# Optimization experiments

Hardware: AMD Instinct MI355X
Metric: run time of the kernel (lower is better)

The kernel has to match this reference:

```python
import jax, jax.numpy as jnp
import numpy as np

SPD_EPS = 1e-3   # added to covariance diagonal
RE_EPS = 1e-4    # ReEig eigenvalue floor


def _semi_orth(key, d_out, d_in):
    # random point on Stiefel manifold: rows orthonormal (d_out <= d_in)
    a = jax.random.normal(key, (d_in, d_out), dtype=jnp.float32)
    q, _ = jnp.linalg.qr(a)          # (d_in, d_out), orthonormal columns
    return q.T                        # (d_out, d_in)


def setup_inputs() -> dict:
    key = jax.random.key(0)
    k_x, k_w1, k_w2, k_fc, k_b = jax.random.split(key, 5)
    B, C, T = 512, 128, 1000
    d1, d2, n_classes = 64, 32, 10
    x = jax.random.normal(k_x, (B, C, T), dtype=jnp.float32)
    W1 = _semi_orth(k_w1, d1, C)          # BiMap 1: (64, 128)
    W2 = _semi_orth(k_w2, d2, d1)         # BiMap 2: (32, 64)
    feat = d2 * d2
    fc_w = jax.random.normal(k_fc, (n_classes, feat), dtype=jnp.float32) / np.sqrt(feat)
    fc_b = jax.random.normal(k_b, (n_classes,), dtype=jnp.float32) * 0.01
    return {"x": x, "W1": W1, "W2": W2, "fc_w": fc_w, "fc_b": fc_b}


def _bimap(S, W):
    # W S W^T, batched: (B,d_in,d_in) -> (B,d_out,d_out)
    return jnp.einsum('ij,bjk,lk->bil', W, S, W)


def _eig_fn(S, fn):
    # eigendecompose symmetric S, apply fn to eigenvalues, reconstruct
    w, V = jnp.linalg.eigh(S)                       # (B,d), (B,d,d)
    return jnp.einsum('bij,bj,bkj->bik', V, fn(w), V)


def reference(x, W1, W2, fc_w, fc_b):
    B, C, T = x.shape
    # per-trial covariance
    x_c = x - x.mean(axis=2, keepdims=True)
    cov = jnp.einsum('bct,bdt->bcd', x_c, x_c) / (T - 1)
    cov = cov + SPD_EPS * jnp.eye(C, dtype=x.dtype)
    # BiMap -> ReEig (x2), then LogEig
    S = _bimap(cov, W1)
    S = _eig_fn(S, lambda w: jnp.maximum(w, RE_EPS))
    S = _bimap(S, W2)
    S = _eig_fn(S, lambda w: jnp.maximum(w, RE_EPS))
    S = _eig_fn(S, jnp.log)
    feats = S.reshape(B, -1)
    return feats @ fc_w.T + fc_b
```

## Files before the change

kernel.cpp:

```cpp
#include <hip/hip_runtime.h>
#include <hip/hip_bf16.h>
#include <math.h>

#define TN 1000
#define SPD_EPS 1e-3f

#define M0 1.16f
#define R0 0.86f
#define BETA 0.7413793103f

typedef float f32x16 __attribute__((ext_vector_type(16)));
typedef short bf16x8 __attribute__((ext_vector_type(8)));

__global__ void w21_kernel(const float* __restrict__ W2, const float* __restrict__ W1,
                           float* __restrict__ W21) {
  int idx = blockIdx.x * 256 + threadIdx.x;
  if (idx < 32 * 128) {
    int c = idx >> 7, k = idx & 127;
    float acc = 0.f;
#pragma unroll 8
    for (int m = 0; m < 64; ++m) acc += W2[c * 64 + m] * W1[m * 128 + k];
    W21[idx] = acc;
  }
}

__device__ __forceinline__ int tix(int r, int c) {
  return r * 4 - (r * (r - 1)) / 2 + (c - r);
}

__global__ __launch_bounds__(256) void cov_kernel(const float* __restrict__ x,
                                                  const float* __restrict__ W21,
                                                  float* __restrict__ S2) {
  const int b = blockIdx.x;
  const int tid = threadIdx.x;
  const int w = tid >> 6;
  const int l = tid & 63;
  const int ch = l & 31;
  const int h = l >> 5;

  __shared__ float Ct[10 * 1056];
  __shared__ float Pl[32 * 130];
  __shared__ float s_part[4][128];
  __shared__ float s_sh[128];

  for (int idx = tid; idx < 10 * 1056; idx += 256) Ct[idx] = 0.f;

  f32x16 acc00{}, acc01{}, acc02{}, acc03{}, acc11{}, acc12{}, acc13{},
         acc22{}, acc23{}, acc33{};
  float s_own[4] = {0.f, 0.f, 0.f, 0.f};
  bf16x8 fr[4];
  const float* xb = x + (size_t)b * (128 * TN) + (size_t)ch * TN + h * 8;
  float4 sa[8], sb[8];
  const float4 z4 = make_float4(0.f, 0.f, 0.f, 0.f);

#define LOADS(ST, KK) do {                                                   \
    const bool v_ = (16 * (KK) + 8 * h) < TN;                                \
    _Pragma("unroll")                                                        \
    for (int r_ = 0; r_ < 4; ++r_) {                                         \
      const float* p_ = xb + r_ * 32 * TN + 16 * (KK);                       \
      float4 t0_ = z4, t1_ = z4;                                             \
      if (v_) { t0_ = *(const float4*)p_; t1_ = *(const float4*)(p_ + 4); }  \
      ST[2 * r_] = t0_; ST[2 * r_ + 1] = t1_;                                \
    } } while (0)

#define CONVS(ST) do {                                                       \
    _Pragma("unroll")                                                        \
    for (int r_ = 0; r_ < 4; ++r_) {                                         \
      union { bf16x8 v; __hip_bfloat16 e[8]; } u_;                           \
      const float f_[8] = {ST[2*r_].x, ST[2*r_].y, ST[2*r_].z, ST[2*r_].w,   \
                           ST[2*r_+1].x, ST[2*r_+1].y, ST[2*r_+1].z,         \
                           ST[2*r_+1].w};                                    \
      float ss_ = 0.f;                                                       \
      _Pragma("unroll")                                                      \
      for (int i_ = 0; i_ < 8; ++i_) {                                       \
        u_.e[i_] = __float2bfloat16(f_[i_]); ss_ += f_[i_];                  \
      }                                                                      \
      fr[r_] = u_.v; s_own[r_] += ss_;                                       \
    } } while (0)

#define MFMAS() do {                                                         \
    acc00 = __builtin_amdgcn_mfma_f32_32x32x16_bf16(fr[0], fr[0], acc00, 0, 0, 0); \
    acc01 = __builtin_amdgcn_mfma_f32_32x32x16_bf16(fr[0], fr[1], acc01, 0, 0, 0); \
    acc02 = __builtin_amdgcn_mfma_f32_32x32x16_bf16(fr[0], fr[2], acc02, 0, 0, 0); \
    acc03 = __builtin_amdgcn_mfma_f32_32x32x16_bf16(fr[0], fr[3], acc03, 0, 0, 0); \
    acc11 = __builtin_amdgcn_mfma_f32_32x32x16_bf16(fr[1], fr[1], acc11, 0, 0, 0); \
    acc12 = __builtin_amdgcn_mfma_f32_32x32x16_bf16(fr[1], fr[2], acc12, 0, 0, 0); \
    acc13 = __builtin_amdgcn_mfma_f32_32x32x16_bf16(fr[1], fr[3], acc13, 0, 0, 0); \
    acc22 = __builtin_amdgcn_mfma_f32_32x32x16_bf16(fr[2], fr[2], acc22, 0, 0, 0); \
    acc23 = __builtin_amdgcn_mfma_f32_32x32x16_bf16(fr[2], fr[3], acc23, 0, 0, 0); \
    acc33 = __builtin_amdgcn_mfma_f32_32x32x16_bf16(fr[3], fr[3], acc33, 0, 0, 0); \
  } while (0)

  LOADS(sa, w);
#pragma unroll 1
  for (int s = w; s < 63; s += 8) {
    LOADS(sb, s + 4); CONVS(sa); MFMAS();
    LOADS(sa, s + 8); CONVS(sb); MFMAS();
  }

#pragma unroll
  for (int r = 0; r < 4; ++r) s_own[r] += __shfl_xor(s_own[r], 32);
  if (h == 0) {
#pragma unroll
    for (int r = 0; r < 4; ++r) s_part[w][32 * r + ch] = s_own[r];
  }
  __syncthreads();
  if (tid < 128)
    s_sh[tid] = s_part[0][tid] + s_part[1][tid] + s_part[2][tid] + s_part[3][tid];

#define ADD_T(ACC_) do {                                                     \
    float* tp_ = Ct + tlc * 1056;                                            \
    _Pragma("unroll")                                                        \
    for (int p_ = 0; p_ < 16; ++p_) {                                        \
      const int row_ = (p_ & 3) + 8 * (p_ >> 2) + 4 * h;                     \
      tp_[row_ * 33 + ch] += ACC_[p_];                                       \
    } } while (0)

#pragma unroll
  for (int s = 0; s < 10; ++s) {
    const int tlc = (s + 3 * w) % 10;
    switch (tlc) {
      case 0: ADD_T(acc00); break;
      case 1: ADD_T(acc01); break;
      case 2: ADD_T(acc02); break;
      case 3: ADD_T(acc03); break;
      case 4: ADD_T(acc11); break;
      case 5: ADD_T(acc12); break;
      case 6: ADD_T(acc13); break;
      case 7: ADD_T(acc22); break;
      case 8: ADD_T(acc23); break;
      case 9: ADD_T(acc33); break;
    }
    __syncthreads();
  }

  {
    const int RB[10] = {0, 0, 0, 0, 1, 1, 1, 2, 2, 3};
    const int CB[10] = {0, 1, 2, 3, 1, 2, 3, 2, 3, 3};
#pragma unroll
    for (int tl = 0; tl < 10; ++tl) {
#pragma unroll
      for (int e0 = 0; e0 < 1024; e0 += 256) {
        const int e = e0 + tid;
        const int row = e >> 5, col = e & 31;
        const int Rg = RB[tl] * 32 + row, Cg = CB[tl] * 32 + col;
        float cv = (Ct[tl * 1056 + row * 33 + col]
                    - s_sh[Rg] * s_sh[Cg] * (1.f / TN)) * (1.f / (TN - 1));
        if (Rg == Cg) cv += SPD_EPS;
        Ct[tl * 1056 + row * 33 + col] = cv;
      }
    }
  }
  __syncthreads();

  {
    const int j = tid & 127;
    const int rh = tid >> 7;
    const int cblk = j >> 5;
    float pa[16];
#pragma unroll
    for (int i = 0; i < 16; ++i) pa[i] = 0.f;
#pragma unroll
    for (int kb = 0; kb < 4; ++kb) {
      const bool up = (kb <= cblk);
      const int t1 = up ? tix(kb, cblk) : tix(cblk, kb);
      const int base = t1 * 1056 + (up ? (j & 31) : (j & 31) * 33);
      const int st = up ? 33 : 1;
      const float* wp = W21 + kb * 32;
#pragma unroll 1
      for (int k2 = 0; k2 < 32; ++k2) {
        const float cv = Ct[base + k2 * st];
#pragma unroll
        for (int i = 0; i < 16; ++i)
          pa[i] = fmaf(wp[(rh * 16 + i) * 128 + k2], cv, pa[i]);
      }
    }
#pragma unroll
    for (int i = 0; i < 16; ++i) Pl[(rh * 16 + i) * 130 + j] = pa[i];
  }
  __syncthreads();

  {
    const int ch2 = tid & 31;
    const int rg = tid >> 5;
    float sc[4] = {0.f, 0.f, 0.f, 0.f};
    const float* wr = W21 + ch2 * 128;
#pragma unroll 1
    for (int k = 0; k < 128; ++k) {
      const float wv = wr[k];
#pragma unroll
      for (int i = 0; i < 4; ++i)
        sc[i] = fmaf(Pl[(rg * 4 + i) * 130 + k], wv, sc[i]);
    }
    float* So = S2 + ((size_t)b << 10);
#pragma unroll
    for (int i = 0; i < 4; ++i) So[(rg * 4 + i) * 32 + ch2] = sc[i];
  }
}

__device__ __forceinline__ void mm_half(float* __restrict__ c,
                                        const float (* __restrict__ A)[36],
                                        const float* __restrict__ bf,
                                        const int r0) {
#pragma unroll 4
  for (int i = 0; i < 16; ++i) {
    const float4* row = (const float4*)(A[r0 + i]);
    float acc = 0.f;
#pragma unroll
    for (int kk = 0; kk < 8; ++kk) {
      const float4 r = row[kk];
      acc = fmaf(r.x, bf[4 * kk + 0], acc);
      acc = fmaf(r.y, bf[4 * kk + 1], acc);
      acc = fmaf(r.z, bf[4 * kk + 2], acc);
      acc = fmaf(r.w, bf[4 * kk + 3], acc);
    }
    c[i] = acc;
  }
}

__device__ __forceinline__ void expand32(float* __restrict__ bf,
                                         const float* __restrict__ v,
                                         const int h) {
#pragma unroll
  for (int i = 0; i < 16; ++i) {
    const float mine = v[i];
    const float other = __shfl_xor(mine, 32);
    bf[i]      = h ? other : mine;
    bf[i + 16] = h ? mine  : other;
  }
}

__global__ __launch_bounds__(64) void logm_fc_kernel(const float* __restrict__ S,
                                                     const float* __restrict__ fcw,
                                                     const float* __restrict__ fcb,
                                                     float* __restrict__ out) {
  const int b = blockIdx.x;
  const int l = threadIdx.x;
  const int j = l & 31;
  const int h = l >> 5;
  const int r0 = h << 4;
  const bool hd = ((j >> 4) == h);
  const int id = j & 15;

  __shared__ float P[6][32][36];
  __shared__ float a_sh[44];

  if (l < 42) {
    if (l == 0) a_sh[0] = logf(M0);
    else a_sh[l] = ((l & 1) ? 1.f : -1.f) * __powf(BETA, (float)l) / (float)l;
  }

  float cur[16], nxt[16], acc[16], bf[32];
  const float* Sb = S + ((size_t)b << 10);
#pragma unroll
  for (int i = 0; i < 16; ++i) {
    float v = Sb[(r0 + i) * 32 + j] * (1.f / R0);
    if (hd && i == id) v -= (M0 / R0);
    cur[i] = v;
    P[0][r0 + i][j] = v;
  }
  __syncthreads();

#pragma unroll 1
  for (int p = 1; p < 6; ++p) {
    expand32(bf, cur, h);
    mm_half(nxt, P[0], bf, r0);
#pragma unroll
    for (int i = 0; i < 16; ++i) { cur[i] = nxt[i]; P[p][r0 + i][j] = nxt[i]; }
  }
  __syncthreads();

#pragma unroll
  for (int i = 0; i < 16; ++i) {
    float v = (hd && i == id) ? a_sh[36] : 0.f;
#pragma unroll
    for (int p = 0; p < 5; ++p)
      v = fmaf(a_sh[37 + p], P[p][r0 + i][j], v);
    acc[i] = v;
  }
#pragma unroll 1
  for (int jj = 5; jj >= 0; --jj) {
    expand32(bf, acc, h);
    mm_half(nxt, P[5], bf, r0);
#pragma unroll
    for (int i = 0; i < 16; ++i) {
      float v = (hd && i == id) ? a_sh[6 * jj] : 0.f;
#pragma unroll
      for (int p = 0; p < 5; ++p)
        v = fmaf(a_sh[6 * jj + 1 + p], P[p][r0 + i][j], v);
      acc[i] = v + nxt[i];
    }
  }

#pragma unroll 2
  for (int k = 0; k < 10; ++k) {
    const float* fw = fcw + (size_t)k * 1024;
    float s = 0.f;
#pragma unroll
    for (int i = 0; i < 16; ++i)
      s = fmaf(acc[i], fw[(r0 + i) * 32 + j], s);
#pragma unroll
    for (int d = 1; d < 64; d <<= 1) s += __shfl_xor(s, d);
    if (l == 0) out[b * 10 + k] = s + fcb[k];
  }
}

extern "C" void kernel_launch(void* const* d_in, const int* in_sizes, int n_in,
                              void* d_out, int out_size, void* d_ws, size_t ws_size,
                              hipStream_t stream) {
  const float* x   = (const float*)d_in[0];
  const float* W1  = (const float*)d_in[1];
  const float* W2  = (const float*)d_in[2];
  const float* fcw = (const float*)d_in[3];
  const float* fcb = (const float*)d_in[4];
  float* out = (float*)d_out;
  char* ws = (char*)d_ws;
  float* W21 = (float*)ws;
  float* S2  = (float*)(ws + 65536);

  w21_kernel<<<16, 256, 0, stream>>>(W2, W1, W21);
  cov_kernel<<<512, 256, 0, stream>>>(x, W21, S2);
  logm_fc_kernel<<<512, 64, 0, stream>>>(S2, fcw, fcb, out);
}
```

Baseline: 171.7 us.

## Stage x tiles through double-buffered LDS with coalesced loads before MFMA covariance

Previously each lane loaded two float4s from per-channel rows in its MFMA fragment layout, so a wavefront touched 32 scattered rows per load. The new code has each wave load 32 full rows of 64-sample chunks with coalesced float4 loads. It converts them to bf16 into a double-buffered LDS tile, computes row sums with shuffles, and then reads MFMA fragments back from LDS. This is meant to improve global memory coalescing and overlap the next chunk's load with MFMA work, at the cost of LDS traffic, a block barrier per chunk, and a shared smem union reused for the covariance tile.

```diff
diff --git a/kernel.cpp b/kernel.cpp
--- a/kernel.cpp
+++ b/kernel.cpp
@@ -28,6 +28,10 @@
   return r * 4 - (r * (r - 1)) / 2 + (c - r);
 }
 
+#define YS_STR 68
+#define YS_ELE (128 * 68)
+#define PL_OFF 42240
+
 __global__ __launch_bounds__(256) void cov_kernel(const float* __restrict__ x,
                                                   const float* __restrict__ W21,
                                                   float* __restrict__ S2) {
@@ -37,45 +41,48 @@
   const int l = tid & 63;
   const int ch = l & 31;
   const int h = l >> 5;
-
-  __shared__ float Ct[10 * 1056];
-  __shared__ float Pl[32 * 130];
-  __shared__ float s_part[4][128];
-  __shared__ float s_sh[128];
-
-  for (int idx = tid; idx < 10 * 1056; idx += 256) Ct[idx] = 0.f;
+  const int g = l & 15;
+  const int rr = l >> 4;
+
+  __shared__ __align__(16) char smem[58880];
+  __shared__ float s_acc[128];
+  ushort* ys = (ushort*)smem;
+  float* Ct = (float*)smem;
+  float* Pl = (float*)(smem + PL_OFF);
+
+  if (tid < 128) s_acc[tid] = 0.f;
 
   f32x16 acc00{}, acc01{}, acc02{}, acc03{}, acc11{}, acc12{}, acc13{},
          acc22{}, acc23{}, acc33{};
-  float s_own[4] = {0.f, 0.f, 0.f, 0.f};
   bf16x8 fr[4];
-  const float* xb = x + (size_t)b * (128 * TN) + (size_t)ch * TN + h * 8;
-  float4 sa[8], sb[8];
+  float4 st[8];
+  const float* xb = x + (size_t)b * (128 * TN);
   const float4 z4 = make_float4(0.f, 0.f, 0.f, 0.f);
 
-#define LOADS(ST, KK) do {                                                   \
-    const bool v_ = (16 * (KK) + 8 * h) < TN;                                \
+#define CLOAD(TT) do {                                                       \
+    const int t0_ = (TT) * 64;                                               \
+    const bool v_ = (4 * g) < (TN - t0_);                                    \
     _Pragma("unroll")                                                        \
-    for (int r_ = 0; r_ < 4; ++r_) {                                         \
-      const float* p_ = xb + r_ * 32 * TN + 16 * (KK);                       \
-      float4 t0_ = z4, t1_ = z4;                                             \
-      if (v_) { t0_ = *(const float4*)p_; t1_ = *(const float4*)(p_ + 4); }  \
-      ST[2 * r_] = t0_; ST[2 * r_ + 1] = t1_;                                \
+    for (int rg_ = 0; rg_ < 8; ++rg_) {                                      \
+      const int R_ = 32 * w + 4 * rg_ + rr;                                  \
+      st[rg_] = v_ ? *(const float4*)(xb + (size_t)R_ * TN + t0_ + 4 * g)    \
+                   : z4;                                                     \
     } } while (0)
 
-#define CONVS(ST) do {                                                       \
+#define CSTORE(BUF) do {                                                     \
+    ushort* yb_ = ys + (BUF) * YS_ELE;                                       \
     _Pragma("unroll")                                                        \
-    for (int r_ = 0; r_ < 4; ++r_) {                                         \
-      union { bf16x8 v; __hip_bfloat16 e[8]; } u_;                           \
-      const float f_[8] = {ST[2*r_].x, ST[2*r_].y, ST[2*r_].z, ST[2*r_].w,   \
-                           ST[2*r_+1].x, ST[2*r_+1].y, ST[2*r_+1].z,         \
-                           ST[2*r_+1].w};                                    \
-      float ss_ = 0.f;                                                       \
-      _Pragma("unroll")                                                      \
-      for (int i_ = 0; i_ < 8; ++i_) {                                       \
-        u_.e[i_] = __float2bfloat16(f_[i_]); ss_ += f_[i_];                  \
-      }                                                                      \
-      fr[r_] = u_.v; s_own[r_] += ss_;                                       \
+    for (int rg_ = 0; rg_ < 8; ++rg_) {                                      \
+      const int R_ = 32 * w + 4 * rg_ + rr;                                  \
+      const float4 v_ = st[rg_];                                             \
+      float sm_ = v_.x + v_.y + v_.z + v_.w;                                 \
+      sm_ += __shfl_xor(sm_, 1); sm_ += __shfl_xor(sm_, 2);                  \
+      sm_ += __shfl_xor(sm_, 4); sm_ += __shfl_xor(sm_, 8);                  \
+      if (g == 0) s_acc[R_] += sm_;                                          \
+      union { ushort4 q; __hip_bfloat16 e[4]; } u_;                          \
+      u_.e[0] = __float2bfloat16(v_.x); u_.e[1] = __float2bfloat16(v_.y);    \
+      u_.e[2] = __float2bfloat16(v_.z); u_.e[3] = __float2bfloat16(v_.w);    \
+      *(ushort4*)(yb_ + R_ * YS_STR + 4 * g) = u_.q;                         \
     } } while (0)
 
 #define MFMAS() do {                                                         \
@@ -91,22 +98,33 @@
     acc33 = __builtin_amdgcn_mfma_f32_32x32x16_bf16(fr[3], fr[3], acc33, 0, 0, 0); \
   } while (0)
 
-  LOADS(sa, w);
-#pragma unroll 1
-  for (int s = w; s < 63; s += 8) {
-    LOADS(sb, s + 4); CONVS(sa); MFMAS();
-    LOADS(sa, s + 8); CONVS(sb); MFMAS();
-  }
-
-#pragma unroll
-  for (int r = 0; r < 4; ++r) s_own[r] += __shfl_xor(s_own[r], 32);
-  if (h == 0) {
-#pragma unroll
-    for (int r = 0; r < 4; ++r) s_part[w][32 * r + ch] = s_own[r];
-  }
-  __syncthreads();
-  if (tid < 128)
-    s_sh[tid] = s_part[0][tid] + s_part[1][tid] + s_part[2][tid] + s_part[3][tid];
+#define CCONSUME(BUF) do {                                                   \
+    const ushort* yb_ = ys + (BUF) * YS_ELE;                                 \
+    const int eb_ = 16 * w + 8 * h;                                          \
+    _Pragma("unroll")                                                        \
+    for (int r_ = 0; r_ < 4; ++r_) {                                         \
+      const ushort* p_ = yb_ + (32 * r_ + ch) * YS_STR + eb_;                \
+      union { ushort4 q[2]; bf16x8 v; } u_;                                  \
+      u_.q[0] = *(const ushort4*)p_;                                         \
+      u_.q[1] = *(const ushort4*)(p_ + 4);                                   \
+      fr[r_] = u_.v;                                                         \
+    }                                                                        \
+    MFMAS(); } while (0)
+
+  CLOAD(0);
+  __syncthreads();
+  CSTORE(0);
+  __syncthreads();
+#pragma unroll 1
+  for (int tt = 0; tt < 16; ++tt) {
+    if (tt < 15) CLOAD(tt + 1);
+    CCONSUME(tt & 1);
+    if (tt < 15) CSTORE((tt + 1) & 1);
+    __syncthreads();
+  }
+
+  for (int idx = tid; idx < 10 * 1056; idx += 256) Ct[idx] = 0.f;
+  __syncthreads();
 
 #define ADD_T(ACC_) do {                                                     \
     float* tp_ = Ct + tlc * 1056;                                            \
@@ -145,7 +163,7 @@
         const int row = e >> 5, col = e & 31;
         const int Rg = RB[tl] * 32 + row, Cg = CB[tl] * 32 + col;
         float cv = (Ct[tl * 1056 + row * 33 + col]
-                    - s_sh[Rg] * s_sh[Cg] * (1.f / TN)) * (1.f / (TN - 1));
+                    - s_acc[Rg] * s_acc[Cg] * (1.f / TN)) * (1.f / (TN - 1));
         if (Rg == Cg) cv += SPD_EPS;
         Ct[tl * 1056 + row * 33 + col] = cv;
       }
@@ -165,11 +183,11 @@
       const bool up = (kb <= cblk);
       const int t1 = up ? tix(kb, cblk) : tix(cblk, kb);
       const int base = t1 * 1056 + (up ? (j & 31) : (j & 31) * 33);
-      const int st = up ? 33 : 1;
+      const int stg = up ? 33 : 1;
       const float* wp = W21 + kb * 32;
 #pragma unroll 1
       for (int k2 = 0; k2 < 32; ++k2) {
-        const float cv = Ct[base + k2 * st];
+        const float cv = Ct[base + k2 * stg];
 #pragma unroll
         for (int i = 0; i < 16; ++i)
           pa[i] = fmaf(wp[(rh * 16 + i) * 128 + k2], cv, pa[i]);
```

Result: faster. 147.6 us (-14.1%).
